# Optimization experiments

Measured on AMD Instinct MI355X. Metric: run time of the kernel, lower is better.

The kernel has to match this reference:

```python
import jax, jax.numpy as jnp
import numpy as np

DIM = 128
CODEBOOK_SCALE = 16384
N_TOKENS = 16384


def setup_inputs() -> dict:
    key = jax.random.key(0)
    k1, k2 = jax.random.split(key)
    x = jax.random.normal(k1, (N_TOKENS, DIM), dtype=jnp.float32)
    codebook = jax.random.normal(k2, (CODEBOOK_SCALE, DIM), dtype=jnp.float32)
    return {"x": x, "codebook": codebook}


def reference(x, codebook):
    # scores: [N, codebook_scale] = x @ codebook.T
    scores = jnp.einsum("nd,cd->nc", x, codebook)
    indices = jnp.argmax(scores, axis=-1)  # [N] int
    loss = jnp.zeros((), dtype=jnp.float32)  # original returns constant 0.0 loss
    return (indices, loss)
```

## Files before the change

### kernel.cpp

```cpp
#include <hip/hip_runtime.h>
#include <hip/hip_bf16.h>

#define NT 16384
#define ND 128
#define NC 16384
#define NSPLIT 8
#define MARGIN 0.4f

typedef __bf16 bf16x8 __attribute__((ext_vector_type(8)));
typedef unsigned short u16x8 __attribute__((ext_vector_type(8)));
typedef float f32x4 __attribute__((ext_vector_type(4)));

#define MF __builtin_amdgcn_mfma_f32_16x16x32_bf16

static __device__ __forceinline__ unsigned short f2bf(float f) {
    unsigned u = __float_as_uint(f);
    return (unsigned short)((u + 0x7FFFu + ((u >> 16) & 1u)) >> 16);
}
static __device__ __forceinline__ float bf2f(unsigned short u) {
    return __uint_as_float(((unsigned)u) << 16);
}
static __device__ __forceinline__ bf16x8 u2b(u16x8 u) {
    return __builtin_bit_cast(bf16x8, u);
}

__global__ __launch_bounds__(256) void lfq_convert_cb(
    const float4* __restrict__ cb4, unsigned short* __restrict__ cbs)
{
    const unsigned i = blockIdx.x * 256 + threadIdx.x;
    const unsigned c  = i >> 4;
    const unsigned k8 = i & 15u;
    const float4 v0 = cb4[i * 2];
    const float4 v1 = cb4[i * 2 + 1];
    const unsigned split = c >> 11;
    const unsigned cl    = c & 2047u;
    const unsigned pair  = cl >> 5;
    const unsigned sp    = (cl >> 4) & 1u;
    const unsigned n     = cl & 15u;
    const unsigned k     = k8 >> 2;
    const unsigned quad  = k8 & 3u;
    const unsigned idx = split * 262144u + pair * 4096u + sp * 2048u +
                         k * 512u + quad * 128u + n * 8u;
    u16x8 h;
    h[0] = f2bf(v0.x); h[1] = f2bf(v0.y); h[2] = f2bf(v0.z); h[3] = f2bf(v0.w);
    h[4] = f2bf(v1.x); h[5] = f2bf(v1.y); h[6] = f2bf(v1.z); h[7] = f2bf(v1.w);
    *(u16x8*)(cbs + idx) = h;
}

static __device__ __forceinline__ float exact_dot(
    const float4* __restrict__ xr4, const float* __restrict__ cf, int cidx)
{
    const float4* cr = (const float4*)(cf + (size_t)cidx * ND);
    float a0 = 0.f, a1 = 0.f, a2 = 0.f, a3 = 0.f;
#pragma unroll
    for (int i = 0; i < 32; i += 4) {
        float4 x0 = xr4[i+0], x1 = xr4[i+1], x2 = xr4[i+2], x3 = xr4[i+3];
        float4 c0 = cr[i+0],  c1 = cr[i+1],  c2 = cr[i+2],  c3 = cr[i+3];
        a0 += x0.x*c0.x + x0.y*c0.y + x0.z*c0.z + x0.w*c0.w;
        a1 += x1.x*c1.x + x1.y*c1.y + x1.z*c1.z + x1.w*c1.w;
        a2 += x2.x*c2.x + x2.y*c2.y + x2.z*c2.z + x2.w*c2.w;
        a3 += x3.x*c3.x + x3.y*c3.y + x3.z*c3.z + x3.w*c3.w;
    }
    return (a0 + a1) + (a2 + a3);
}

static __device__ __forceinline__ float exact_dot_g(
    const float* __restrict__ xf, const float* __restrict__ cf,
    int token, int cidx)
{
    const float4* xr = (const float4*)(xf + (size_t)token * ND);
    const float4* cr = (const float4*)(cf + (size_t)cidx * ND);
    float a0 = 0.f, a1 = 0.f, a2 = 0.f, a3 = 0.f;
#pragma unroll
    for (int i = 0; i < 32; i += 4) {
        float4 x0 = xr[i+0], x1 = xr[i+1], x2 = xr[i+2], x3 = xr[i+3];
        float4 c0 = cr[i+0], c1 = cr[i+1], c2 = cr[i+2], c3 = cr[i+3];
        a0 += x0.x*c0.x + x0.y*c0.y + x0.z*c0.z + x0.w*c0.w;
        a1 += x1.x*c1.x + x1.y*c1.y + x1.z*c1.z + x1.w*c1.w;
        a2 += x2.x*c2.x + x2.y*c2.y + x2.z*c2.z + x2.w*c2.w;
        a3 += x3.x*c3.x + x3.y*c3.y + x3.z*c3.z + x3.w*c3.w;
    }
    return (a0 + a1) + (a2 + a3);
}

static __device__ __forceinline__ void top2_upd(
    const f32x4& a, float* b1r, float* b2r, unsigned pk)
{
#pragma unroll
    for (int r4 = 0; r4 < 4; ++r4) {
        float p = __uint_as_float((__float_as_uint(a[r4]) & 0xFFFFFF80u) | pk);
        b2r[r4] = __builtin_amdgcn_fmed3f(p, b1r[r4], b2r[r4]);
        b1r[r4] = fmaxf(p, b1r[r4]);
    }
}

__global__ __launch_bounds__(256)
__attribute__((amdgpu_waves_per_eu(2, 2)))
void lfq_stage1(
    const float* __restrict__ xf, const unsigned short* __restrict__ cbs,
    float* __restrict__ sb1, float* __restrict__ sb2,
    int* __restrict__ si1, int* __restrict__ si2)
{
    const int split = blockIdx.x & 7;
    const int tb    = blockIdx.x >> 3;
    const int t0    = tb * 256;
    const int tid   = threadIdx.x;
    const int w     = tid >> 6;
    const int lane  = tid & 63;
    const int n     = lane & 15;
    const int quad  = lane >> 4;

    bf16x8 ah[4][4];
#pragma unroll
    for (int tt = 0; tt < 4; ++tt) {
        const float* xr = xf + (size_t)(t0 + w * 64 + tt * 16 + n) * ND + quad * 8;
#pragma unroll
        for (int kk = 0; kk < 4; ++kk) {
            float4 v0 = *(const float4*)(xr + kk * 32);
            float4 v1 = *(const float4*)(xr + kk * 32 + 4);
            u16x8 hu;
            hu[0] = f2bf(v0.x);
            hu[1] = f2bf(v0.y);
            hu[2] = f2bf(v0.z);
            hu[3] = f2bf(v0.w);
            hu[4] = f2bf(v1.x);
            hu[5] = f2bf(v1.y);
            hu[6] = f2bf(v1.z);
            hu[7] = f2bf(v1.w);
            ah[tt][kk] = u2b(hu);
        }
    }

    float b1[4][4], b2[4][4];
#pragma unroll
    for (int tt = 0; tt < 4; ++tt)
#pragma unroll
        for (int r = 0; r < 4; ++r) { b1[tt][r] = -3.0e38f; b2[tt][r] = -3.0e38f; }

    const unsigned char* gp =
        (const unsigned char*)cbs + (size_t)split * 524288u +
        (unsigned)lane * 16u;

    const f32x4 zq = {0.f, 0.f, 0.f, 0.f};

#define LOADPAIR(Q0,Q1,Q2,Q3,Q4,Q5,Q6,Q7, G)                                   \
    Q0 = *(const bf16x8*)((G));                                                \
    Q1 = *(const bf16x8*)((G) + 1024);                                         \
    Q2 = *(const bf16x8*)((G) + 2048);                                         \
    Q3 = *(const bf16x8*)((G) + 3072);                                         \
    Q4 = *(const bf16x8*)((G) + 4096);                                         \
    Q5 = *(const bf16x8*)((G) + 5120);                                         \
    Q6 = *(const bf16x8*)((G) + 6144);                                         \
    Q7 = *(const bf16x8*)((G) + 7168);

#define COMPUTE(Q0,Q1,Q2,Q3,Q4,Q5,Q6,Q7, P)                                    \
    {                                                                          \
        f32x4 aA0, aA1, aA2, aA3, aB0, aB1, aB2, aB3;                          \
        __builtin_amdgcn_s_setprio(1);                                         \
        aA0 = MF(ah[0][0], Q0, zq,  0,0,0);                                    \
        aA1 = MF(ah[1][0], Q0, zq,  0,0,0);                                    \
        aA2 = MF(ah[2][0], Q0, zq,  0,0,0);                                    \
        aA3 = MF(ah[3][0], Q0, zq,  0,0,0);                                    \
        aB0 = MF(ah[0][0], Q4, zq,  0,0,0);                                    \
        aB1 = MF(ah[1][0], Q4, zq,  0,0,0);                                    \
        aB2 = MF(ah[2][0], Q4, zq,  0,0,0);                                    \
        aB3 = MF(ah[3][0], Q4, zq,  0,0,0);                                    \
        aA0 = MF(ah[0][1], Q1, aA0, 0,0,0);                                    \
        aA1 = MF(ah[1][1], Q1, aA1, 0,0,0);                                    \
        aA2 = MF(ah[2][1], Q1, aA2, 0,0,0);                                    \
        aA3 = MF(ah[3][1], Q1, aA3, 0,0,0);                                    \
        aB0 = MF(ah[0][1], Q5, aB0, 0,0,0);                                    \
        aB1 = MF(ah[1][1], Q5, aB1, 0,0,0);                                    \
        aB2 = MF(ah[2][1], Q5, aB2, 0,0,0);                                    \
        aB3 = MF(ah[3][1], Q5, aB3, 0,0,0);                                    \
        aA0 = MF(ah[0][2], Q2, aA0, 0,0,0);                                    \
        aA1 = MF(ah[1][2], Q2, aA1, 0,0,0);                                    \
        aA2 = MF(ah[2][2], Q2, aA2, 0,0,0);                                    \
        aA3 = MF(ah[3][2], Q2, aA3, 0,0,0);                                    \
        aB0 = MF(ah[0][2], Q6, aB0, 0,0,0);                                    \
        aB1 = MF(ah[1][2], Q6, aB1, 0,0,0);                                    \
        aB2 = MF(ah[2][2], Q6, aB2, 0,0,0);                                    \
        aB3 = MF(ah[3][2], Q6, aB3, 0,0,0);                                    \
        aA0 = MF(ah[0][3], Q3, aA0, 0,0,0);                                    \
        aA1 = MF(ah[1][3], Q3, aA1, 0,0,0);                                    \
        aA2 = MF(ah[2][3], Q3, aA2, 0,0,0);                                    \
        aA3 = MF(ah[3][3], Q3, aA3, 0,0,0);                                    \
        aB0 = MF(ah[0][3], Q7, aB0, 0,0,0);                                    \
        aB1 = MF(ah[1][3], Q7, aB1, 0,0,0);                                    \
        aB2 = MF(ah[2][3], Q7, aB2, 0,0,0);                                    \
        aB3 = MF(ah[3][3], Q7, aB3, 0,0,0);                                    \
        __builtin_amdgcn_s_setprio(0);                                         \
        const unsigned pkA = (unsigned)(127 - (P) * 2);                        \
        const unsigned pkB = (unsigned)(127 - (P) * 2 - 1);                    \
        top2_upd(aA0, b1[0], b2[0], pkA);                                      \
        top2_upd(aA1, b1[1], b2[1], pkA);                                      \
        top2_upd(aA2, b1[2], b2[2], pkA);                                      \
        top2_upd(aA3, b1[3], b2[3], pkA);                                      \
        top2_upd(aB0, b1[0], b2[0], pkB);                                      \
        top2_upd(aB1, b1[1], b2[1], pkB);                                      \
        top2_upd(aB2, b1[2], b2[2], pkB);                                      \
        top2_upd(aB3, b1[3], b2[3], pkB);                                      \
    }

    bf16x8 qa0, qa1, qa2, qa3, qa4, qa5, qa6, qa7;
    bf16x8 qb0, qb1, qb2, qb3, qb4, qb5, qb6, qb7;

    LOADPAIR(qa0,qa1,qa2,qa3,qa4,qa5,qa6,qa7, gp)

    {
        const unsigned slot = __builtin_amdgcn_s_getreg(6148) & 3u;
        for (unsigned i = 0; i < slot; ++i) __builtin_amdgcn_s_sleep(30);
    }

    for (int p = 0; p < 62; p += 2) {
        LOADPAIR(qb0,qb1,qb2,qb3,qb4,qb5,qb6,qb7, gp + (p + 1) * 8192)
        COMPUTE (qa0,qa1,qa2,qa3,qa4,qa5,qa6,qa7, p)
        LOADPAIR(qa0,qa1,qa2,qa3,qa4,qa5,qa6,qa7, gp + (p + 2) * 8192)
        COMPUTE (qb0,qb1,qb2,qb3,qb4,qb5,qb6,qb7, p + 1)
    }
    LOADPAIR(qb0,qb1,qb2,qb3,qb4,qb5,qb6,qb7, gp + 63 * 8192)
    COMPUTE (qa0,qa1,qa2,qa3,qa4,qa5,qa6,qa7, 62)
    COMPUTE (qb0,qb1,qb2,qb3,qb4,qb5,qb6,qb7, 63)

#undef LOADPAIR
#undef COMPUTE

    const int cb_base = split * (NC / NSPLIT);
    float v1[4][4], v2[4][4];
    int   c1[4][4], c2[4][4];
#pragma unroll
    for (int tt = 0; tt < 4; ++tt)
#pragma unroll
        for (int r = 0; r < 4; ++r) {
            int j1 = 127 - (int)(__float_as_uint(b1[tt][r]) & 127u);
            int j2 = 127 - (int)(__float_as_uint(b2[tt][r]) & 127u);
            v1[tt][r] = b1[tt][r]; c1[tt][r] = cb_base + j1 * 16 + n;
            v2[tt][r] = b2[tt][r]; c2[tt][r] = cb_base + j2 * 16 + n;
        }

#pragma unroll
    for (int tt = 0; tt < 4; ++tt)
#pragma unroll
        for (int r = 0; r < 4; ++r) {
#pragma unroll
            for (int off = 1; off < 16; off <<= 1) {
                float ob1 = __shfl_xor(v1[tt][r], off, 64);
                int   oi1 = __shfl_xor(c1[tt][r], off, 64);
                float ob2 = __shfl_xor(v2[tt][r], off, 64);
                int   oi2 = __shfl_xor(c2[tt][r], off, 64);
                bool gt = (ob1 > v1[tt][r]) ||
                          (ob1 == v1[tt][r] && oi1 < c1[tt][r]);
                float ls = gt ? v1[tt][r] : ob1;
                int   li = gt ? c1[tt][r] : oi1;
                float ws_ = gt ? ob2 : v2[tt][r];
                int   wi = gt ? oi2 : c2[tt][r];
                bool s2 = (ls > ws_) || (ls == ws_ && li < wi);
                v2[tt][r] = s2 ? ls : ws_;
                c2[tt][r] = s2 ? li : wi;
                v1[tt][r] = gt ? ob1 : v1[tt][r];
                c1[tt][r] = gt ? oi1 : c1[tt][r];
            }
        }

    if (n == 0) {
#pragma unroll
        for (int tt = 0; tt < 4; ++tt)
#pragma unroll
            for (int r = 0; r < 4; ++r) {
                const int token = t0 + w * 64 + tt * 16 + quad * 4 + r;
                const size_t o = (size_t)split * NT + token;
                sb1[o] = v1[tt][r]; si1[o] = c1[tt][r];
                sb2[o] = v2[tt][r]; si2[o] = c2[tt][r];
            }
    }
}

__global__ __launch_bounds__(256) void lfq_combine(
    const float* __restrict__ sb1, const float* __restrict__ sb2,
    const int* __restrict__ si1, const int* __restrict__ si2,
    const float* __restrict__ xf, const float* __restrict__ cf,
    float* __restrict__ out, int out_size)
{
    const int lane = threadIdx.x & 63;
    const int wv   = threadIdx.x >> 6;
    const int g    = lane >> 3;
    const int cl   = lane & 7;
    const int t    = (blockIdx.x * 4 + wv) * 8 + g;

    const size_t o = (size_t)cl * NT + t;
    const float va = sb1[o]; const int ia = si1[o];
    const float vb = sb2[o]; const int ib = si2[o];

    bool lgt = (vb > va) || (vb == va && ib < ia);
    float m  = lgt ? vb : va;
    int   mi = lgt ? ib : ia;
#pragma unroll
    for (int off = 1; off < 8; off <<= 1) {
        float om = __shfl_xor(m, off, 64);
        int   oi = __shfl_xor(mi, off, 64);
        if (om > m || (om == m && oi < mi)) { m = om; mi = oi; }
    }
    const float A1 = m;
    const int   I1 = mi;

    const bool ba = (va >= A1 - MARGIN);
    const bool bb_ = (vb >= A1 - MARGIN);
    int cnt = (ba ? 1 : 0) + (bb_ ? 1 : 0);
#pragma unroll
    for (int off = 1; off < 8; off <<= 1)
        cnt += __shfl_xor(cnt, off, 64);

    int bi = I1;
    if (cnt > 1) {
        float sa = -__builtin_inff(), sb_ = -__builtin_inff();
        if (ba)  sa  = exact_dot_g(xf, cf, t, ia);
        if (bb_) sb_ = exact_dot_g(xf, cf, t, ib);
        bool g2 = (sb_ > sa) || (sb_ == sa && ib < ia);
        float bs = g2 ? sb_ : sa;
        int  bid = g2 ? ib : ia;
#pragma unroll
        for (int off = 1; off < 8; off <<= 1) {
            float os = __shfl_xor(bs, off, 64);
            int   oi = __shfl_xor(bid, off, 64);
            if (os > bs || (os == bs && oi < bid)) { bs = os; bid = oi; }
        }
        bi = bid;
    }
    if (cl == 0) out[t] = (float)bi;
    if (blockIdx.x == 0 && threadIdx.x == 0 && out_size > NT) out[NT] = 0.0f;
}

__global__ __launch_bounds__(512) void lfq_fp32_argmax(
    const float* __restrict__ xf, const float* __restrict__ cf,
    float* __restrict__ out, int out_size)
{
    const int tid = threadIdx.x;
    const int w   = tid >> 6;
    const int tok = tid & 63;
    const int t0  = blockIdx.x * 64;
    __shared__ float s_sc[8][64];
    __shared__ int   s_ix[8][64];

    float4 xr[32];
    const float4* xrow = (const float4*)(xf + (size_t)(t0 + tok) * ND);
#pragma unroll
    for (int i = 0; i < 32; ++i) xr[i] = xrow[i];

    float bs = -__builtin_inff();
    int   bi = 0;
    const int c_begin = w * (NC / 8);
    for (int c = c_begin; c < c_begin + NC / 8; ++c) {
        float s = exact_dot(xr, cf, c);
        if (s > bs) { bs = s; bi = c; }
    }
    s_sc[w][tok] = bs; s_ix[w][tok] = bi;
    __syncthreads();
    if (tid < 64) {
        float bsf = s_sc[0][tid]; int bif = s_ix[0][tid];
#pragma unroll
        for (int ww = 1; ww < 8; ++ww) {
            float s2 = s_sc[ww][tid]; int ii = s_ix[ww][tid];
            if (s2 > bsf || (s2 == bsf && ii < bif)) { bsf = s2; bif = ii; }
        }
        out[t0 + tid] = (float)bif;
    }
    if (blockIdx.x == 0 && tid == 0 && out_size > NT) out[NT] = 0.0f;
}

extern "C" void kernel_launch(void* const* d_in, const int* in_sizes, int n_in,
                              void* d_out, int out_size, void* d_ws, size_t ws_size,
                              hipStream_t stream) {
    const float* x  = (const float*)d_in[0];
    const float* cb = (const float*)d_in[1];
    float* out = (float*)d_out;

    const size_t NCE = (size_t)NC * ND;
    const size_t NEED = NCE * 2 + (size_t)NT * NSPLIT * 4 * 4;
    if (ws_size >= NEED) {
        char* ws = (char*)d_ws;
        unsigned short* cbs = (unsigned short*)ws;
        char* sp = ws + NCE * 2;
        float* sb1 = (float*)sp;
        float* sb2 = (float*)(sp + (size_t)NT * NSPLIT * 4);
        int*   si1 = (int*)  (sp + (size_t)NT * NSPLIT * 8);
        int*   si2 = (int*)  (sp + (size_t)NT * NSPLIT * 12);

        lfq_convert_cb<<<dim3(1024), dim3(256), 0, stream>>>(
            (const float4*)cb, cbs);
        lfq_stage1<<<dim3((NT / 256) * NSPLIT), dim3(256), 0, stream>>>(
            x, cbs, sb1, sb2, si1, si2);
        lfq_combine<<<dim3(NT / 32), dim3(256), 0, stream>>>(
            sb1, sb2, si1, si2, x, cb, out, out_size);
    } else {
        lfq_fp32_argmax<<<dim3(NT / 64), dim3(512), 0, stream>>>(x, cb, out, out_size);
    }
}
```

Measured before the change: 158.3 us.

## Software-pipeline top-2 screening of previous tile under current MFMA chain

```diff
diff --git a/kernel.cpp b/kernel.cpp
--- a/kernel.cpp
+++ b/kernel.cpp
@@ -11,7 +11,8 @@
 typedef unsigned short u16x8 __attribute__((ext_vector_type(8)));
 typedef float f32x4 __attribute__((ext_vector_type(4)));
 
-#define MF __builtin_amdgcn_mfma_f32_16x16x32_bf16
+#define MF  __builtin_amdgcn_mfma_f32_16x16x32_bf16
+#define SGB __builtin_amdgcn_sched_group_barrier
 
 static __device__ __forceinline__ unsigned short f2bf(float f) {
     unsigned u = __float_as_uint(f);
@@ -143,87 +144,146 @@
 
     const f32x4 zq = {0.f, 0.f, 0.f, 0.f};
 
-#define LOADPAIR(Q0,Q1,Q2,Q3,Q4,Q5,Q6,Q7, G)                                   \
-    Q0 = *(const bf16x8*)((G));                                                \
-    Q1 = *(const bf16x8*)((G) + 1024);                                         \
-    Q2 = *(const bf16x8*)((G) + 2048);                                         \
-    Q3 = *(const bf16x8*)((G) + 3072);                                         \
-    Q4 = *(const bf16x8*)((G) + 4096);                                         \
-    Q5 = *(const bf16x8*)((G) + 5120);                                         \
-    Q6 = *(const bf16x8*)((G) + 6144);                                         \
-    Q7 = *(const bf16x8*)((G) + 7168);
-
-#define COMPUTE(Q0,Q1,Q2,Q3,Q4,Q5,Q6,Q7, P)                                    \
+#define LOADP(Q, G)                                                            \
+    Q##0 = *(const bf16x8*)((G));                                              \
+    Q##1 = *(const bf16x8*)((G) + 1024);                                       \
+    Q##2 = *(const bf16x8*)((G) + 2048);                                       \
+    Q##3 = *(const bf16x8*)((G) + 3072);                                       \
+    Q##4 = *(const bf16x8*)((G) + 4096);                                       \
+    Q##5 = *(const bf16x8*)((G) + 5120);                                       \
+    Q##6 = *(const bf16x8*)((G) + 6144);                                       \
+    Q##7 = *(const bf16x8*)((G) + 7168);
+
+#define COMPUTE0(AC, Q)                                                        \
+    AC##0 = MF(ah[0][0], Q##0, zq,   0,0,0);                                   \
+    AC##1 = MF(ah[1][0], Q##0, zq,   0,0,0);                                   \
+    AC##2 = MF(ah[2][0], Q##0, zq,   0,0,0);                                   \
+    AC##3 = MF(ah[3][0], Q##0, zq,   0,0,0);                                   \
+    AC##4 = MF(ah[0][0], Q##4, zq,   0,0,0);                                   \
+    AC##5 = MF(ah[1][0], Q##4, zq,   0,0,0);                                   \
+    AC##6 = MF(ah[2][0], Q##4, zq,   0,0,0);                                   \
+    AC##7 = MF(ah[3][0], Q##4, zq,   0,0,0);                                   \
+    AC##0 = MF(ah[0][1], Q##1, AC##0, 0,0,0);                                  \
+    AC##1 = MF(ah[1][1], Q##1, AC##1, 0,0,0);                                  \
+    AC##2 = MF(ah[2][1], Q##1, AC##2, 0,0,0);                                  \
+    AC##3 = MF(ah[3][1], Q##1, AC##3, 0,0,0);                                  \
+    AC##4 = MF(ah[0][1], Q##5, AC##4, 0,0,0);                                  \
+    AC##5 = MF(ah[1][1], Q##5, AC##5, 0,0,0);                                  \
+    AC##6 = MF(ah[2][1], Q##5, AC##6, 0,0,0);                                  \
+    AC##7 = MF(ah[3][1], Q##5, AC##7, 0,0,0);                                  \
+    AC##0 = MF(ah[0][2], Q##2, AC##0, 0,0,0);                                  \
+    AC##1 = MF(ah[1][2], Q##2, AC##1, 0,0,0);                                  \
+    AC##2 = MF(ah[2][2], Q##2, AC##2, 0,0,0);                                  \
+    AC##3 = MF(ah[3][2], Q##2, AC##3, 0,0,0);                                  \
+    AC##4 = MF(ah[0][2], Q##6, AC##4, 0,0,0);                                  \
+    AC##5 = MF(ah[1][2], Q##6, AC##5, 0,0,0);                                  \
+    AC##6 = MF(ah[2][2], Q##6, AC##6, 0,0,0);                                  \
+    AC##7 = MF(ah[3][2], Q##6, AC##7, 0,0,0);                                  \
+    AC##0 = MF(ah[0][3], Q##3, AC##0, 0,0,0);                                  \
+    AC##1 = MF(ah[1][3], Q##3, AC##1, 0,0,0);                                  \
+    AC##2 = MF(ah[2][3], Q##3, AC##2, 0,0,0);                                  \
+    AC##3 = MF(ah[3][3], Q##3, AC##3, 0,0,0);                                  \
+    AC##4 = MF(ah[0][3], Q##7, AC##4, 0,0,0);                                  \
+    AC##5 = MF(ah[1][3], Q##7, AC##5, 0,0,0);                                  \
+    AC##6 = MF(ah[2][3], Q##7, AC##6, 0,0,0);                                  \
+    AC##7 = MF(ah[3][3], Q##7, AC##7, 0,0,0);
+
+#define COMPUTE(AC, Q, SC, PPREV)                                              \
     {                                                                          \
-        f32x4 aA0, aA1, aA2, aA3, aB0, aB1, aB2, aB3;                          \
-        __builtin_amdgcn_s_setprio(1);                                         \
-        aA0 = MF(ah[0][0], Q0, zq,  0,0,0);                                    \
-        aA1 = MF(ah[1][0], Q0, zq,  0,0,0);                                    \
-        aA2 = MF(ah[2][0], Q0, zq,  0,0,0);                                    \
-        aA3 = MF(ah[3][0], Q0, zq,  0,0,0);                                    \
-        aB0 = MF(ah[0][0], Q4, zq,  0,0,0);                                    \
-        aB1 = MF(ah[1][0], Q4, zq,  0,0,0);                                    \
-        aB2 = MF(ah[2][0], Q4, zq,  0,0,0);                                    \
-        aB3 = MF(ah[3][0], Q4, zq,  0,0,0);                                    \
-        aA0 = MF(ah[0][1], Q1, aA0, 0,0,0);                                    \
-        aA1 = MF(ah[1][1], Q1, aA1, 0,0,0);                                    \
-        aA2 = MF(ah[2][1], Q1, aA2, 0,0,0);                                    \
-        aA3 = MF(ah[3][1], Q1, aA3, 0,0,0);                                    \
-        aB0 = MF(ah[0][1], Q5, aB0, 0,0,0);                                    \
-        aB1 = MF(ah[1][1], Q5, aB1, 0,0,0);                                    \
-        aB2 = MF(ah[2][1], Q5, aB2, 0,0,0);                                    \
-        aB3 = MF(ah[3][1], Q5, aB3, 0,0,0);                                    \
-        aA0 = MF(ah[0][2], Q2, aA0, 0,0,0);                                    \
-        aA1 = MF(ah[1][2], Q2, aA1, 0,0,0);                                    \
-        aA2 = MF(ah[2][2], Q2, aA2, 0,0,0);                                    \
-        aA3 = MF(ah[3][2], Q2, aA3, 0,0,0);                                    \
-        aB0 = MF(ah[0][2], Q6, aB0, 0,0,0);                                    \
-        aB1 = MF(ah[1][2], Q6, aB1, 0,0,0);                                    \
-        aB2 = MF(ah[2][2], Q6, aB2, 0,0,0);                                    \
-        aB3 = MF(ah[3][2], Q6, aB3, 0,0,0);                                    \
-        aA0 = MF(ah[0][3], Q3, aA0, 0,0,0);                                    \
-        aA1 = MF(ah[1][3], Q3, aA1, 0,0,0);                                    \
-        aA2 = MF(ah[2][3], Q3, aA2, 0,0,0);                                    \
-        aA3 = MF(ah[3][3], Q3, aA3, 0,0,0);                                    \
-        aB0 = MF(ah[0][3], Q7, aB0, 0,0,0);                                    \
-        aB1 = MF(ah[1][3], Q7, aB1, 0,0,0);                                    \
-        aB2 = MF(ah[2][3], Q7, aB2, 0,0,0);                                    \
-        aB3 = MF(ah[3][3], Q7, aB3, 0,0,0);                                    \
-        __builtin_amdgcn_s_setprio(0);                                         \
+        const unsigned pkA = (unsigned)(127 - (PPREV) * 2);                    \
+        const unsigned pkB = (unsigned)(127 - (PPREV) * 2 - 1);                \
+        AC##0 = MF(ah[0][0], Q##0, zq,   0,0,0);                               \
+        AC##1 = MF(ah[1][0], Q##0, zq,   0,0,0);                               \
+        AC##2 = MF(ah[2][0], Q##0, zq,   0,0,0);                               \
+        AC##3 = MF(ah[3][0], Q##0, zq,   0,0,0);                               \
+        AC##4 = MF(ah[0][0], Q##4, zq,   0,0,0);                               \
+        AC##5 = MF(ah[1][0], Q##4, zq,   0,0,0);                               \
+        AC##6 = MF(ah[2][0], Q##4, zq,   0,0,0);                               \
+        AC##7 = MF(ah[3][0], Q##4, zq,   0,0,0);                               \
+        SGB(0x8, 8, 0);                                                        \
+        top2_upd(SC##0, b1[0], b2[0], pkA);                                    \
+        top2_upd(SC##1, b1[1], b2[1], pkA);                                    \
+        SGB(0x2, 32, 0);                                                       \
+        AC##0 = MF(ah[0][1], Q##1, AC##0, 0,0,0);                              \
+        AC##1 = MF(ah[1][1], Q##1, AC##1, 0,0,0);                              \
+        AC##2 = MF(ah[2][1], Q##1, AC##2, 0,0,0);                              \
+        AC##3 = MF(ah[3][1], Q##1, AC##3, 0,0,0);                              \
+        AC##4 = MF(ah[0][1], Q##5, AC##4, 0,0,0);                              \
+        AC##5 = MF(ah[1][1], Q##5, AC##5, 0,0,0);                              \
+        AC##6 = MF(ah[2][1], Q##5, AC##6, 0,0,0);                              \
+        AC##7 = MF(ah[3][1], Q##5, AC##7, 0,0,0);                              \
+        SGB(0x8, 8, 0);                                                        \
+        top2_upd(SC##2, b1[2], b2[2], pkA);                                    \
+        top2_upd(SC##3, b1[3], b2[3], pkA);                                    \
+        SGB(0x2, 32, 0);                                                       \
+        AC##0 = MF(ah[0][2], Q##2, AC##0, 0,0,0);                              \
+        AC##1 = MF(ah[1][2], Q##2, AC##1, 0,0,0);                              \
+        AC##2 = MF(ah[2][2], Q##2, AC##2, 0,0,0);                              \
+        AC##3 = MF(ah[3][2], Q##2, AC##3, 0,0,0);                              \
+        AC##4 = MF(ah[0][2], Q##6, AC##4, 0,0,0);                              \
+        AC##5 = MF(ah[1][2], Q##6, AC##5, 0,0,0);                              \
+        AC##6 = MF(ah[2][2], Q##6, AC##6, 0,0,0);                              \
+        AC##7 = MF(ah[3][2], Q##6, AC##7, 0,0,0);                              \
+        SGB(0x8, 8, 0);                                                        \
+        top2_upd(SC##4, b1[0], b2[0], pkB);                                    \
+        top2_upd(SC##5, b1[1], b2[1], pkB);                                    \
+        SGB(0x2, 32, 0);                                                       \
+        AC##0 = MF(ah[0][3], Q##3, AC##0, 0,0,0);                              \
+        AC##1 = MF(ah[1][3], Q##3, AC##1, 0,0,0);                              \
+        AC##2 = MF(ah[2][3], Q##3, AC##2, 0,0,0);                              \
+        AC##3 = MF(ah[3][3], Q##3, AC##3, 0,0,0);                              \
+        AC##4 = MF(ah[0][3], Q##7, AC##4, 0,0,0);                              \
+        AC##5 = MF(ah[1][3], Q##7, AC##5, 0,0,0);                              \
+        AC##6 = MF(ah[2][3], Q##7, AC##6, 0,0,0);                              \
+        AC##7 = MF(ah[3][3], Q##7, AC##7, 0,0,0);                              \
+        SGB(0x8, 8, 0);                                                        \
+        top2_upd(SC##6, b1[2], b2[2], pkB);                                    \
+        top2_upd(SC##7, b1[3], b2[3], pkB);                                    \
+        SGB(0x2, 32, 0);                                                       \
+    }
+
+#define SCREEN(SC, P)                                                          \
+    {                                                                          \
         const unsigned pkA = (unsigned)(127 - (P) * 2);                        \
         const unsigned pkB = (unsigned)(127 - (P) * 2 - 1);                    \
-        top2_upd(aA0, b1[0], b2[0], pkA);                                      \
-        top2_upd(aA1, b1[1], b2[1], pkA);                                      \
-        top2_upd(aA2, b1[2], b2[2], pkA);                                      \
-        top2_upd(aA3, b1[3], b2[3], pkA);                                      \
-        top2_upd(aB0, b1[0], b2[0], pkB);                                      \
-        top2_upd(aB1, b1[1], b2[1], pkB);                                      \
-        top2_upd(aB2, b1[2], b2[2], pkB);                                      \
-        top2_upd(aB3, b1[3], b2[3], pkB);                                      \
+        top2_upd(SC##0, b1[0], b2[0], pkA);                                    \
+        top2_upd(SC##1, b1[1], b2[1], pkA);                                    \
+        top2_upd(SC##2, b1[2], b2[2], pkA);                                    \
+        top2_upd(SC##3, b1[3], b2[3], pkA);                                    \
+        top2_upd(SC##4, b1[0], b2[0], pkB);                                    \
+        top2_upd(SC##5, b1[1], b2[1], pkB);                                    \
+        top2_upd(SC##6, b1[2], b2[2], pkB);                                    \
+        top2_upd(SC##7, b1[3], b2[3], pkB);                                    \
     }
 
     bf16x8 qa0, qa1, qa2, qa3, qa4, qa5, qa6, qa7;
     bf16x8 qb0, qb1, qb2, qb3, qb4, qb5, qb6, qb7;
-
-    LOADPAIR(qa0,qa1,qa2,qa3,qa4,qa5,qa6,qa7, gp)
+    f32x4 U0, U1, U2, U3, U4, U5, U6, U7;
+    f32x4 V0, V1, V2, V3, V4, V5, V6, V7;
+
+    LOADP(qa, gp)
 
     {
         const unsigned slot = __builtin_amdgcn_s_getreg(6148) & 3u;
         for (unsigned i = 0; i < slot; ++i) __builtin_amdgcn_s_sleep(30);
     }
 
-    for (int p = 0; p < 62; p += 2) {
-        LOADPAIR(qb0,qb1,qb2,qb3,qb4,qb5,qb6,qb7, gp + (p + 1) * 8192)
-        COMPUTE (qa0,qa1,qa2,qa3,qa4,qa5,qa6,qa7, p)
-        LOADPAIR(qa0,qa1,qa2,qa3,qa4,qa5,qa6,qa7, gp + (p + 2) * 8192)
-        COMPUTE (qb0,qb1,qb2,qb3,qb4,qb5,qb6,qb7, p + 1)
-    }
-    LOADPAIR(qb0,qb1,qb2,qb3,qb4,qb5,qb6,qb7, gp + 63 * 8192)
-    COMPUTE (qa0,qa1,qa2,qa3,qa4,qa5,qa6,qa7, 62)
-    COMPUTE (qb0,qb1,qb2,qb3,qb4,qb5,qb6,qb7, 63)
-
-#undef LOADPAIR
+    LOADP(qb, gp + 8192)
+    COMPUTE0(U, qa)
+
+    for (int p = 1; p < 63; p += 2) {
+        LOADP(qa, gp + (p + 1) * 8192)
+        COMPUTE(V, qb, U, p - 1)
+        LOADP(qb, gp + (p + 2) * 8192)
+        COMPUTE(U, qa, V, p)
+    }
+    COMPUTE(V, qb, U, 62)
+    SCREEN(V, 63)
+
+#undef LOADP
+#undef COMPUTE0
 #undef COMPUTE
+#undef SCREEN
 
     const int cb_base = split * (NC / NSPLIT);
     float v1[4][4], v2[4][4];
```

Result: slower. 174.2 us (+10.0%).
